# Kernel optimization log

Measured on AMD Instinct MI355X. Metric: run time of the kernel, lower is better.

## Reference

```python
import jax, jax.numpy as jnp
import numpy as np

HIDDEN = 2048
NUM_HEADS = 32
NUM_KV_HEADS = 8
HEAD_DIM = HIDDEN // NUM_HEADS  # 64
GROUP = NUM_HEADS // NUM_KV_HEADS  # 4
B, S = 2, 2048


def setup_inputs() -> dict:
    key = jax.random.key(0)
    ks = jax.random.split(key, 9)
    sc = 0.02
    kv_dim = NUM_KV_HEADS * HEAD_DIM
    return {
        "x": jax.random.normal(ks[0], (B, S, HIDDEN), jnp.float32),
        # weights stored as [in, out] (transpose of torch Linear.weight)
        "Wq": jax.random.normal(ks[1], (HIDDEN, HIDDEN), jnp.float32) * sc,
        "bq": jnp.zeros((HIDDEN,), jnp.float32),
        "Wk": jax.random.normal(ks[2], (HIDDEN, kv_dim), jnp.float32) * sc,
        "bk": jnp.zeros((kv_dim,), jnp.float32),
        "Wv": jax.random.normal(ks[3], (HIDDEN, kv_dim), jnp.float32) * sc,
        "bv": jnp.zeros((kv_dim,), jnp.float32),
        "Wo": jax.random.normal(ks[4], (HIDDEN, HIDDEN), jnp.float32) * sc,
        "bo": jnp.zeros((HIDDEN,), jnp.float32),
    }


def reference(x, Wq, bq, Wk, bk, Wv, bv, Wo, bo):
    b, s, _ = x.shape
    q = (x @ Wq + bq).reshape(b, s, NUM_KV_HEADS, GROUP, HEAD_DIM)
    k = (x @ Wk + bk).reshape(b, s, NUM_KV_HEADS, HEAD_DIM)
    v = (x @ Wv + bv).reshape(b, s, NUM_KV_HEADS, HEAD_DIM)
    scale = 1.0 / jnp.sqrt(jnp.asarray(HEAD_DIM, x.dtype))
    # scores: [b, g(kv heads), r(q per group), s(query), t(key)]
    scores = jnp.einsum("bsgrd,btgd->bgrst", q, k) * scale
    attn = jax.nn.softmax(scores, axis=-1)  # dropout rate 0 -> identity
    out = jnp.einsum("bgrst,btgd->bsgrd", attn, v).reshape(b, s, HIDDEN)
    return out @ Wo + bo
```

## Files before the change

kernel.cpp:

```cpp
#include <hip/hip_runtime.h>

#define HIDDEN 2048
#define NHEADS 32
#define NKV 8
#define HD 64
#define BATCH 2
#define SEQ 2048
#define KVD 512
#define BSZ 4096
#define QKVD 3072

typedef __bf16 bfx8 __attribute__((ext_vector_type(8)));
typedef __bf16 bfx4 __attribute__((ext_vector_type(4)));
typedef __bf16 bfx2 __attribute__((ext_vector_type(2)));
typedef float f32x4 __attribute__((ext_vector_type(4)));
typedef unsigned int ux4 __attribute__((ext_vector_type(4)));

#define QSCALE 0.1803368801111204f

__device__ __forceinline__ void gl_lds16(const __bf16* g, __bf16* l) {
    __builtin_amdgcn_global_load_lds(
        (const __attribute__((address_space(1))) unsigned int*)g,
        (__attribute__((address_space(3))) unsigned int*)l, 16, 0, 0);
}

__device__ __forceinline__ unsigned int pk2(float lo, float hi) {
    bfx2 v = {(__bf16)lo, (__bf16)hi};
    return __builtin_bit_cast(unsigned int, v);
}

__global__ __launch_bounds__(256) void cvt_bf16(const float* __restrict__ src,
                                                __bf16* __restrict__ dst, int n4) {
    int i = blockIdx.x * 256 + threadIdx.x;
    if (i >= n4) return;
    float4 f = ((const float4*)src)[i];
    bfx4 o = {(__bf16)f.x, (__bf16)f.y, (__bf16)f.z, (__bf16)f.w};
    *(bfx4*)(dst + (size_t)i * 4) = o;
}

__device__ __forceinline__ void tcvt_tile(const float* __restrict__ src,
                                          __bf16* __restrict__ dst,
                                          int R, int C, int tx, int ty,
                                          float (*tile)[65], int t, float mul) {
    int br = ty * 64, bc = tx * 64;
    {
        int r = t >> 4, c = (t & 15) * 4;
#pragma unroll
        for (int i = 0; i < 4; ++i) {
            float4 v = *(const float4*)(&src[(long)(br + r + i * 16) * C + bc + c]);
            tile[r + i * 16][c + 0] = v.x * mul;
            tile[r + i * 16][c + 1] = v.y * mul;
            tile[r + i * 16][c + 2] = v.z * mul;
            tile[r + i * 16][c + 3] = v.w * mul;
        }
    }
    __syncthreads();
    {
        int d = t >> 2, tt0 = (t & 3) * 16;
        bfx8 o0, o1;
#pragma unroll
        for (int j = 0; j < 8; ++j) o0[j] = (__bf16)tile[tt0 + j][d];
#pragma unroll
        for (int j = 0; j < 8; ++j) o1[j] = (__bf16)tile[tt0 + 8 + j][d];
        *(bfx8*)(&dst[(long)(bc + d) * R + br + tt0]) = o0;
        *(bfx8*)(&dst[(long)(bc + d) * R + br + tt0 + 8]) = o1;
    }
}

__global__ __launch_bounds__(256) void prep(const float* __restrict__ Wq,
                                            const float* __restrict__ Wk,
                                            const float* __restrict__ Wv,
                                            const float* __restrict__ Wo,
                                            const float* __restrict__ bq,
                                            const float* __restrict__ bk,
                                            const float* __restrict__ bv,
                                            __bf16* __restrict__ wqkvt,
                                            __bf16* __restrict__ wot,
                                            float* __restrict__ bqkv) {
    __shared__ float tile[64][65];
    int idx = blockIdx.x, t = threadIdx.x;
    if (idx < 1024) {
        tcvt_tile(Wq, wqkvt, HIDDEN, HIDDEN, idx & 31, idx >> 5, tile, t, QSCALE);
    } else if (idx < 1280) {
        int l = idx - 1024;
        tcvt_tile(Wk, wqkvt + (size_t)HIDDEN * HIDDEN, HIDDEN, KVD, l & 7, l >> 3, tile, t, 1.0f);
    } else if (idx < 1536) {
        int l = idx - 1280;
        tcvt_tile(Wv, wqkvt + (size_t)(HIDDEN + KVD) * HIDDEN, HIDDEN, KVD, l & 7, l >> 3, tile, t, 1.0f);
    } else if (idx < 2560) {
        int l = idx - 1536;
        tcvt_tile(Wo, wot, HIDDEN, HIDDEN, l & 31, l >> 5, tile, t, 1.0f);
    } else {
        int i = (idx - 2560) * 256 + t;
        if (i < QKVD) {
            float v = (i < HIDDEN) ? bq[i] * QSCALE
                                   : (i < HIDDEN + KVD ? bk[i - HIDDEN] : bv[i - HIDDEN - KVD]);
            bqkv[i] = v;
        }
    }
}

__global__ __launch_bounds__(256) void transpose_v(const __bf16* __restrict__ qkv,
                                                   __bf16* __restrict__ vt) {
    __shared__ __bf16 tile[64][65];
    int t = threadIdx.x;
    int nb0 = blockIdx.x * 64;
    int bh = blockIdx.y;
    int b = bh >> 3, kv = bh & 7;
    {
        int tt = t >> 2, c0 = (t & 3) * 16;
        const __bf16* p = &qkv[(long)(b * SEQ + nb0 + tt) * QKVD + HIDDEN + KVD + kv * HD + c0];
        bfx8 a0 = *(const bfx8*)(p);
        bfx8 a1 = *(const bfx8*)(p + 8);
#pragma unroll
        for (int j = 0; j < 8; ++j) tile[tt][c0 + j] = a0[j];
#pragma unroll
        for (int j = 0; j < 8; ++j) tile[tt][c0 + 8 + j] = a1[j];
    }
    __syncthreads();
    {
        int d = t >> 2, tt0 = (t & 3) * 16;
        bfx8 o0, o1;
#pragma unroll
        for (int j = 0; j < 8; ++j) o0[j] = tile[tt0 + j][d];
#pragma unroll
        for (int j = 0; j < 8; ++j) o1[j] = tile[tt0 + 8 + j][d];
        __bf16* q = &vt[((long)bh * HD + d) * SEQ + nb0 + tt0];
        *(bfx8*)(q) = o0;
        *(bfx8*)(q + 8) = o1;
    }
}

template <bool OUT_BF16>
__global__ __launch_bounds__(256, 3) void gemm128(const __bf16* __restrict__ A,
                                                  const __bf16* __restrict__ Bt,
                                                  const float* __restrict__ bias,
                                                  void* __restrict__ C,
                                                  int M, int N, int K) {
    __shared__ __align__(16) __bf16 As[2][128 * 32];
    __shared__ __align__(16) __bf16 Bs[2][128 * 32];
    int t = threadIdx.x;
    int w = t >> 6, lane = t & 63;
    int lrow = lane & 15, quad = lane >> 4;
    long m0 = (long)blockIdx.y * 128, n0 = (long)blockIdx.x * 128;
    int wr = (w >> 1) * 64, wc = (w & 1) * 64;
    f32x4 acc[4][4] = {};
    int srow = t >> 2, scol = (((t & 3) ^ ((t >> 3) & 3))) * 8;
    int sA = (lrow >> 1) & 3;
    const __bf16* Ag = A + (m0 + srow) * (long)K + scol;
    const __bf16* Bg = Bt + (n0 + srow) * (long)K + scol;
#define STAGE_G(kb, buf)                                                      \
    {                                                                         \
        _Pragma("unroll") for (int c = 0; c < 2; ++c) {                       \
            gl_lds16(Ag + (long)c * 64 * K + (kb), &As[buf][c * 2048 + w * 512]); \
            gl_lds16(Bg + (long)c * 64 * K + (kb), &Bs[buf][c * 2048 + w * 512]); \
        }                                                                     \
    }
    STAGE_G(0, 0);
    int nk = K >> 5;
    for (int it = 0; it < nk; ++it) {
        __syncthreads();
        if (it + 1 < nk) STAGE_G((it + 1) * 32, (it + 1) & 1);
        const __bf16* Ab = &As[it & 1][0];
        const __bf16* Bb = &Bs[it & 1][0];
        bfx8 af[4], bfr[4];
#pragma unroll
        for (int i = 0; i < 4; ++i)
            af[i] = *(const bfx8*)&Ab[(wr + i * 16 + lrow) * 32 + ((quad ^ sA) * 8)];
#pragma unroll
        for (int j = 0; j < 4; ++j)
            bfr[j] = *(const bfx8*)&Bb[(wc + j * 16 + lrow) * 32 + ((quad ^ sA) * 8)];
#pragma unroll
        for (int i = 0; i < 4; ++i)
#pragma unroll
            for (int j = 0; j < 4; ++j)
                acc[i][j] = __builtin_amdgcn_mfma_f32_16x16x32_bf16(af[i], bfr[j], acc[i][j], 0, 0, 0);
    }
#undef STAGE_G
#pragma unroll
    for (int j = 0; j < 4; ++j) {
        long col = n0 + wc + j * 16 + lrow;
        float bv = bias[col];
#pragma unroll
        for (int i = 0; i < 4; ++i) {
#pragma unroll
            for (int r = 0; r < 4; ++r) {
                long row = m0 + wr + i * 16 + quad * 4 + r;
                float val = acc[i][j][r] + bv;
                if (OUT_BF16)
                    ((__bf16*)C)[row * N + col] = (__bf16)val;
                else
                    ((float*)C)[row * N + col] = val;
            }
        }
    }
}

__global__ __launch_bounds__(256, 4) void attn(const __bf16* __restrict__ QKV,
                                               const __bf16* __restrict__ Vt,
                                               __bf16* __restrict__ O) {
    __shared__ __align__(16) __bf16 Ks[2][64 * 64];
    __shared__ __align__(16) __bf16 Vs[2][64 * 64];
    int t = threadIdx.x;
    int w = t >> 6, lane = t & 63;
    int lrow = lane & 15, quad = lane >> 4;
    int qb = blockIdx.x, bh = blockIdx.y;
    int b = bh >> 5, h = bh & 31, kv = h >> 2;
    int q0 = qb * 128 + w * 32;

    bfx8 qf[2][2];
#pragma unroll
    for (int i = 0; i < 2; ++i)
#pragma unroll
        for (int kk = 0; kk < 2; ++kk)
            qf[i][kk] = *(const bfx8*)(QKV + (long)(b * SEQ + q0 + i * 16 + lrow) * QKVD +
                                       h * HD + kk * 32 + quad * 8);

    int srow = t >> 2, scol = (((t & 3) ^ ((t >> 3) & 3))) * 8;
    int sA = (lrow >> 1) & 3;
    const __bf16* kg = QKV + (long)(b * SEQ + srow) * QKVD + HIDDEN + kv * HD + scol;
    const __bf16* vg = Vt + ((long)(b * NKV + kv) * HD + srow) * SEQ + scol;
#define STAGE_KV(nb, buf)                                                          \
    {                                                                              \
        _Pragma("unroll") for (int c = 0; c < 2; ++c) {                            \
            gl_lds16(kg + (long)(nb)*QKVD + c * 32, &Ks[buf][c * 2048 + w * 512]); \
            gl_lds16(vg + (nb) + c * 32, &Vs[buf][c * 2048 + w * 512]);            \
        }                                                                          \
    }
    STAGE_KV(0, 0);

    f32x4 accO[4][2] = {};
    float lacc[2] = {0.f, 0.f};

    for (int it = 0; it < SEQ / 64; ++it) {
        __syncthreads();
        if (it + 1 < SEQ / 64) STAGE_KV((it + 1) * 64, (it + 1) & 1);
        const __bf16* Kb = &Ks[it & 1][0];
        const __bf16* Vb = &Vs[it & 1][0];
#pragma unroll
        for (int ch = 0; ch < 2; ++ch) {
            f32x4 s2[2][2];
#pragma unroll
            for (int tp = 0; tp < 2; ++tp) {
                int tt = ch * 2 + tp;
                bfx8 ka0 = *(const bfx8*)&Kb[tt * 512 + lrow * 32 + ((quad ^ sA) * 8)];
                bfx8 ka1 = *(const bfx8*)&Kb[2048 + tt * 512 + lrow * 32 + ((quad ^ sA) * 8)];
                __builtin_amdgcn_s_setprio(1);
#pragma unroll
                for (int i = 0; i < 2; ++i) {
                    f32x4 z = {};
                    z = __builtin_amdgcn_mfma_f32_16x16x32_bf16(ka0, qf[i][0], z, 0, 0, 0);
                    s2[tp][i] = __builtin_amdgcn_mfma_f32_16x16x32_bf16(ka1, qf[i][1], z, 0, 0, 0);
                }
                __builtin_amdgcn_s_setprio(0);
            }
            bfx8 p8v[2];
#pragma unroll
            for (int i = 0; i < 2; ++i) {
                float pa0 = __builtin_amdgcn_exp2f(s2[0][i][0]);
                float pa1 = __builtin_amdgcn_exp2f(s2[0][i][1]);
                float pa2 = __builtin_amdgcn_exp2f(s2[0][i][2]);
                float pa3 = __builtin_amdgcn_exp2f(s2[0][i][3]);
                float pb0 = __builtin_amdgcn_exp2f(s2[1][i][0]);
                float pb1 = __builtin_amdgcn_exp2f(s2[1][i][1]);
                float pb2 = __builtin_amdgcn_exp2f(s2[1][i][2]);
                float pb3 = __builtin_amdgcn_exp2f(s2[1][i][3]);
                lacc[i] += ((pa0 + pa1) + (pa2 + pa3)) + ((pb0 + pb1) + (pb2 + pb3));
                unsigned int A0 = pk2(pa0, pa1), A1 = pk2(pa2, pa3);
                unsigned int B0 = pk2(pb0, pb1), B1 = pk2(pb2, pb3);
                asm("v_permlane32_swap_b32 %0, %1" : "+v"(A0), "+v"(B0));
                asm("v_permlane16_swap_b32 %0, %1" : "+v"(A0), "+v"(B0));
                asm("v_permlane32_swap_b32 %0, %1" : "+v"(A1), "+v"(B1));
                asm("v_permlane16_swap_b32 %0, %1" : "+v"(A1), "+v"(B1));
                ux4 pw = {A0, A1, B0, B1};
                p8v[i] = __builtin_bit_cast(bfx8, pw);
            }
#pragma unroll
            for (int dt = 0; dt < 4; ++dt) {
                bfx8 va = *(const bfx8*)&Vb[ch * 2048 + (dt * 16 + lrow) * 32 + ((quad ^ sA) * 8)];
                __builtin_amdgcn_s_setprio(1);
#pragma unroll
                for (int i = 0; i < 2; ++i)
                    accO[dt][i] = __builtin_amdgcn_mfma_f32_16x16x32_bf16(va, p8v[i], accO[dt][i], 0, 0, 0);
                __builtin_amdgcn_s_setprio(0);
            }
        }
    }
    float inv[2];
#pragma unroll
    for (int i = 0; i < 2; ++i) {
        float l = lacc[i];
        l += __shfl_xor(l, 16);
        l += __shfl_xor(l, 32);
        inv[i] = 1.0f / l;
    }
#pragma unroll
    for (int i = 0; i < 2; ++i) {
        long row = (long)(b * SEQ + q0 + i * 16 + lrow);
#pragma unroll
        for (int dt = 0; dt < 4; ++dt) {
            bfx4 o4 = {(__bf16)(accO[dt][i][0] * inv[i]), (__bf16)(accO[dt][i][1] * inv[i]),
                       (__bf16)(accO[dt][i][2] * inv[i]), (__bf16)(accO[dt][i][3] * inv[i])};
            *(bfx4*)&O[row * HIDDEN + h * HD + dt * 16 + quad * 4] = o4;
        }
    }
#undef STAGE_KV
}

extern "C" void kernel_launch(void* const* d_in, const int* in_sizes, int n_in,
                              void* d_out, int out_size, void* d_ws, size_t ws_size,
                              hipStream_t stream) {
    const float* x  = (const float*)d_in[0];
    const float* Wq = (const float*)d_in[1];
    const float* bq = (const float*)d_in[2];
    const float* Wk = (const float*)d_in[3];
    const float* bk = (const float*)d_in[4];
    const float* Wv = (const float*)d_in[5];
    const float* bv = (const float*)d_in[6];
    const float* Wo = (const float*)d_in[7];
    const float* bo = (const float*)d_in[8];
    float* out = (float*)d_out;

    __bf16* ws    = (__bf16*)d_ws;
    __bf16* xb    = ws;
    __bf16* wqkvt = xb + (size_t)BSZ * HIDDEN;
    __bf16* wot   = wqkvt + (size_t)QKVD * HIDDEN;
    __bf16* qkv   = wot + (size_t)HIDDEN * HIDDEN;
    __bf16* vt_   = qkv + (size_t)BSZ * QKVD;
    __bf16* ab_   = vt_ + (size_t)BSZ * KVD;
    float*  bqkv  = (float*)(ab_ + (size_t)BSZ * HIDDEN);

    cvt_bf16<<<(BSZ * HIDDEN / 4 + 255) / 256, 256, 0, stream>>>(x, xb, BSZ * HIDDEN / 4);
    prep<<<2560 + (QKVD + 255) / 256, 256, 0, stream>>>(Wq, Wk, Wv, Wo, bq, bk, bv,
                                                        wqkvt, wot, bqkv);

    gemm128<true><<<dim3(QKVD / 128, BSZ / 128), 256, 0, stream>>>(xb, wqkvt, bqkv, qkv, BSZ, QKVD, HIDDEN);

    transpose_v<<<dim3(SEQ / 64, BATCH * NKV), 256, 0, stream>>>(qkv, vt_);
    attn<<<dim3(SEQ / 128, BATCH * NHEADS), 256, 0, stream>>>(qkv, vt_, ab_);

    gemm128<false><<<dim3(HIDDEN / 128, BSZ / 128), 256, 0, stream>>>(ab_, wot, bo, out, BSZ, HIDDEN, HIDDEN);
}
```

Baseline: 317.2 us.

## Fuse x conversion into prep and write transposed V from QKV GEMM epilogue

Folds the fp32-to-bf16 conversion of x into the prep kernel as extra blocks, and has the QKV GEMM write its V columns directly in transposed layout. This removes the cvt_bf16 and transpose_v launches and the extra global round trip for V. The V epilogue stores 4-element bf16 vectors strided by SEQ, which may be less coalesced than the row-major stores.

```diff
diff --git a/kernel.cpp b/kernel.cpp
--- a/kernel.cpp
+++ b/kernel.cpp
@@ -29,15 +29,6 @@
     return __builtin_bit_cast(unsigned int, v);
 }
 
-__global__ __launch_bounds__(256) void cvt_bf16(const float* __restrict__ src,
-                                                __bf16* __restrict__ dst, int n4) {
-    int i = blockIdx.x * 256 + threadIdx.x;
-    if (i >= n4) return;
-    float4 f = ((const float4*)src)[i];
-    bfx4 o = {(__bf16)f.x, (__bf16)f.y, (__bf16)f.z, (__bf16)f.w};
-    *(bfx4*)(dst + (size_t)i * 4) = o;
-}
-
 __device__ __forceinline__ void tcvt_tile(const float* __restrict__ src,
                                           __bf16* __restrict__ dst,
                                           int R, int C, int tx, int ty,
@@ -67,13 +58,15 @@
     }
 }
 
-__global__ __launch_bounds__(256) void prep(const float* __restrict__ Wq,
+__global__ __launch_bounds__(256) void prep(const float* __restrict__ x,
+                                            const float* __restrict__ Wq,
                                             const float* __restrict__ Wk,
                                             const float* __restrict__ Wv,
                                             const float* __restrict__ Wo,
                                             const float* __restrict__ bq,
                                             const float* __restrict__ bk,
                                             const float* __restrict__ bv,
+                                            __bf16* __restrict__ xb,
                                             __bf16* __restrict__ wqkvt,
                                             __bf16* __restrict__ wot,
                                             float* __restrict__ bqkv) {
@@ -90,52 +83,27 @@
     } else if (idx < 2560) {
         int l = idx - 1536;
         tcvt_tile(Wo, wot, HIDDEN, HIDDEN, l & 31, l >> 5, tile, t, 1.0f);
-    } else {
+    } else if (idx < 2572) {
         int i = (idx - 2560) * 256 + t;
         if (i < QKVD) {
             float v = (i < HIDDEN) ? bq[i] * QSCALE
                                    : (i < HIDDEN + KVD ? bk[i - HIDDEN] : bv[i - HIDDEN - KVD]);
             bqkv[i] = v;
         }
-    }
-}
-
-__global__ __launch_bounds__(256) void transpose_v(const __bf16* __restrict__ qkv,
-                                                   __bf16* __restrict__ vt) {
-    __shared__ __bf16 tile[64][65];
-    int t = threadIdx.x;
-    int nb0 = blockIdx.x * 64;
-    int bh = blockIdx.y;
-    int b = bh >> 3, kv = bh & 7;
-    {
-        int tt = t >> 2, c0 = (t & 3) * 16;
-        const __bf16* p = &qkv[(long)(b * SEQ + nb0 + tt) * QKVD + HIDDEN + KVD + kv * HD + c0];
-        bfx8 a0 = *(const bfx8*)(p);
-        bfx8 a1 = *(const bfx8*)(p + 8);
-#pragma unroll
-        for (int j = 0; j < 8; ++j) tile[tt][c0 + j] = a0[j];
-#pragma unroll
-        for (int j = 0; j < 8; ++j) tile[tt][c0 + 8 + j] = a1[j];
-    }
-    __syncthreads();
-    {
-        int d = t >> 2, tt0 = (t & 3) * 16;
-        bfx8 o0, o1;
-#pragma unroll
-        for (int j = 0; j < 8; ++j) o0[j] = tile[tt0 + j][d];
-#pragma unroll
-        for (int j = 0; j < 8; ++j) o1[j] = tile[tt0 + 8 + j][d];
-        __bf16* q = &vt[((long)bh * HD + d) * SEQ + nb0 + tt0];
-        *(bfx8*)(q) = o0;
-        *(bfx8*)(q + 8) = o1;
-    }
-}
-
-template <bool OUT_BF16>
+    } else {
+        int i = (idx - 2572) * 256 + t;
+        float4 f = ((const float4*)x)[i];
+        bfx4 o = {(__bf16)f.x, (__bf16)f.y, (__bf16)f.z, (__bf16)f.w};
+        *(bfx4*)(xb + (size_t)i * 4) = o;
+    }
+}
+
+template <bool OUT_BF16, bool VSPLIT>
 __global__ __launch_bounds__(256, 3) void gemm128(const __bf16* __restrict__ A,
                                                   const __bf16* __restrict__ Bt,
                                                   const float* __restrict__ bias,
                                                   void* __restrict__ C,
+                                                  __bf16* __restrict__ vt,
                                                   int M, int N, int K) {
     __shared__ __align__(16) __bf16 As[2][128 * 32];
     __shared__ __align__(16) __bf16 Bs[2][128 * 32];
@@ -177,6 +145,22 @@
                 acc[i][j] = __builtin_amdgcn_mfma_f32_16x16x32_bf16(af[i], bfr[j], acc[i][j], 0, 0, 0);
     }
 #undef STAGE_G
+    if (VSPLIT && n0 >= (long)(HIDDEN + KVD)) {
+        int b = (int)(m0 >> 11);
+        int s0 = (int)(m0 & 2047) + wr + quad * 4;
+#pragma unroll
+        for (int j = 0; j < 4; ++j) {
+            int off = (int)(n0 - (HIDDEN + KVD)) + wc + j * 16 + lrow;
+            float bv = bias[n0 + wc + j * 16 + lrow];
+#pragma unroll
+            for (int i = 0; i < 4; ++i) {
+                bfx4 o4 = {(__bf16)(acc[i][j][0] + bv), (__bf16)(acc[i][j][1] + bv),
+                           (__bf16)(acc[i][j][2] + bv), (__bf16)(acc[i][j][3] + bv)};
+                *(bfx4*)&vt[((long)b * KVD + off) * SEQ + s0 + i * 16] = o4;
+            }
+        }
+        return;
+    }
 #pragma unroll
     for (int j = 0; j < 4; ++j) {
         long col = n0 + wc + j * 16 + lrow;
@@ -330,14 +314,14 @@
     __bf16* ab_   = vt_ + (size_t)BSZ * KVD;
     float*  bqkv  = (float*)(ab_ + (size_t)BSZ * HIDDEN);
 
-    cvt_bf16<<<(BSZ * HIDDEN / 4 + 255) / 256, 256, 0, stream>>>(x, xb, BSZ * HIDDEN / 4);
-    prep<<<2560 + (QKVD + 255) / 256, 256, 0, stream>>>(Wq, Wk, Wv, Wo, bq, bk, bv,
-                                                        wqkvt, wot, bqkv);
-
-    gemm128<true><<<dim3(QKVD / 128, BSZ / 128), 256, 0, stream>>>(xb, wqkvt, bqkv, qkv, BSZ, QKVD, HIDDEN);
-
-    transpose_v<<<dim3(SEQ / 64, BATCH * NKV), 256, 0, stream>>>(qkv, vt_);
+    prep<<<2572 + 8192, 256, 0, stream>>>(x, Wq, Wk, Wv, Wo, bq, bk, bv,
+                                          xb, wqkvt, wot, bqkv);
+
+    gemm128<true, true><<<dim3(QKVD / 128, BSZ / 128), 256, 0, stream>>>(
+        xb, wqkvt, bqkv, qkv, vt_, BSZ, QKVD, HIDDEN);
+
     attn<<<dim3(SEQ / 128, BATCH * NHEADS), 256, 0, stream>>>(qkv, vt_, ab_);
 
-    gemm128<false><<<dim3(HIDDEN / 128, BSZ / 128), 256, 0, stream>>>(ab_, wot, bo, out, BSZ, HIDDEN, HIDDEN);
-}
+    gemm128<false, false><<<dim3(HIDDEN / 128, BSZ / 128), 256, 0, stream>>>(
+        ab_, wot, (const float*)bo, out, nullptr, BSZ, HIDDEN, HIDDEN);
+}
```

New measurement: 312.7 us. No clear change (-1.4%).
